# Kernel optimization log

Hardware: AMD Instinct MI355X
Metric: run time of the kernel (lower is better)

The kernel has to match this reference:

```python
import jax, jax.numpy as jnp
import numpy as np
from jax import lax

C_IN, C_OUT, K = 32, 64, 3
SUPPORT_LEN, ORDER = 1, 2
GC_IN = (ORDER * SUPPORT_LEN + 1) * C_IN  # 96
N, V, T = 32, 500, 96


def _conv2d_1xk(x, w, b):
    # x: (N,C,V,T), w: (O,I,1,K), valid padding -> (N,O,V,T-K+1)
    y = lax.conv_general_dilated(x, w, window_strides=(1, 1), padding='VALID',
                                 dimension_numbers=('NCHW', 'OIHW', 'NCHW'))
    return y + b[None, :, None, None]


def setup_inputs() -> dict:
    key = jax.random.key(0)
    ks = jax.random.split(key, 12)
    x = jax.random.normal(ks[0], (N, C_IN, V, T), dtype=jnp.float32)
    A = jax.random.uniform(ks[1], (V, V), dtype=jnp.float32)
    A = A / jnp.sum(A, axis=1, keepdims=True)  # random-walk normalization
    s = 1.0 / np.sqrt(C_IN * K)
    w1 = jax.random.uniform(ks[2], (C_IN, C_IN, 1, K), jnp.float32, -s, s)
    b1 = jax.random.uniform(ks[3], (C_IN,), jnp.float32, -s, s)
    w2 = jax.random.uniform(ks[4], (C_IN, C_IN, 1, K), jnp.float32, -s, s)
    b2 = jax.random.uniform(ks[5], (C_IN,), jnp.float32, -s, s)
    w3 = jax.random.uniform(ks[6], (C_IN, C_IN, 1, K), jnp.float32, -s, s)
    b3 = jax.random.uniform(ks[7], (C_IN,), jnp.float32, -s, s)
    so = 1.0 / np.sqrt(GC_IN)
    w_out = jax.random.uniform(ks[8], (C_OUT, GC_IN), jnp.float32, -so, so)
    b_out = jax.random.uniform(ks[9], (C_OUT,), jnp.float32, -so, so)
    prelu_a = jnp.asarray(0.25, dtype=jnp.float32)
    return {"x": x, "A": A, "w1": w1, "b1": b1, "w2": w2, "b2": b2,
            "w3": w3, "b3": b3, "w_out": w_out, "b_out": b_out,
            "prelu_a": prelu_a}


def reference(x, A, w1, b1, w2, b2, w3, b3, w_out, b_out, prelu_a):
    # TimeBlock: gated temporal conv with residual-relu
    temp = _conv2d_1xk(x, w1, b1) + jax.nn.sigmoid(_conv2d_1xk(x, w2, b2))
    xt = jax.nn.relu(temp + _conv2d_1xk(x, w3, b3))  # (N,C,V,T-2)
    # gcn: multi-hop diffusion, order=2, single support
    x1 = jnp.einsum('ncvl,vw->ncwl', xt, A)
    x2 = jnp.einsum('ncvl,vw->ncwl', x1, A)
    h = jnp.concatenate([xt, x1, x2], axis=1)  # (N,3C,V,T-2)
    # 1x1 conv projection
    out = jnp.einsum('ncvl,oc->novl', h, w_out) + b_out[None, :, None, None]
    # PReLU (scalar parameter); dropout is a no-op (training=self.training, eval)
    out = jnp.where(out > 0, out, prelu_a * out)
    return out
```

## Files before the change

### kernel.cpp

```cpp
#include <hip/hip_runtime.h>
#include <stdint.h>


typedef float  f32x4  __attribute__((ext_vector_type(4)));
typedef float  f32x2  __attribute__((ext_vector_type(2)));
typedef short  bf16x8 __attribute__((ext_vector_type(8)));

static __device__ __forceinline__ unsigned short f2bf(float f) {
    union { float f; unsigned u; } v; v.f = f;
    unsigned u = v.u;
    return (unsigned short)((u + 0x7fffu + ((u >> 16) & 1u)) >> 16);
}

#define WS_S   ((size_t)1024 * 64 * 96 * 8 * 2)
#define AT_B   (512u * 512u * 2u)
#define WA_B   (3u * 96u * 32u * 2u)

static __device__ __forceinline__ int swz(int row, int q) {
    return q ^ (row & 3) ^ ((row >> 2) & 3);
}

__global__ __launch_bounds__(256)
void prep_kernel(const float* __restrict__ A,
                 const float* __restrict__ w1, const float* __restrict__ w2,
                 const float* __restrict__ w3, const float* __restrict__ wout,
                 unsigned short* __restrict__ At, unsigned short* __restrict__ Wa,
                 unsigned short* __restrict__ Wo)
{
    int idx = blockIdx.x * 256 + threadIdx.x;
    if (idx < 512 * 512) {
        int w = idx >> 9, v = idx & 511;
        float val = (w < 500 && v < 500) ? A[v * 500 + w] : 0.f;
        At[idx] = f2bf(val);
    } else if (idx < 512 * 512 + 3 * 3 * 32 * 32) {
        int t = idx - 512 * 512;
        int ci = t & 31;
        int co = (t >> 5) & 31;
        int rc = t >> 10;
        int conv = rc % 3, koff = rc / 3;
        const float* ws = (conv == 0) ? w1 : ((conv == 1) ? w2 : w3);
        Wa[t] = f2bf(ws[co * 96 + ci * 3 + koff]);
    } else if (idx < 512 * 512 + 3 * 3 * 32 * 32 + 64 * 96) {
        int t = idx - (512 * 512 + 3 * 3 * 32 * 32);
        Wo[t] = f2bf(wout[t]);
    }
}

__global__ __launch_bounds__(512, 1)
void conv_kernel(const float* __restrict__ x, const unsigned short* __restrict__ Wa,
                 const float* __restrict__ b1, const float* __restrict__ b2,
                 const float* __restrict__ b3, unsigned short* __restrict__ xt)
{
    __shared__ unsigned short Xs2[52 * 256];
    __shared__ unsigned short WaSh[9216];
    __shared__ unsigned short stash[32 * 408];

    const int th   = blockIdx.x;
    const int vblk = blockIdx.y;
    const int n    = blockIdx.z;
    const int tid  = threadIdx.x;
    const int lane = tid & 63, wv = tid >> 6;
    const int cl = lane & 15, q4 = lane >> 4;
    const int nbase = wv * 48;

    for (int g = tid; g < 1152; g += 512)
        *(uint4*)&WaSh[g * 8] = *(const uint4*)(Wa + g * 8);

    for (int s = 0; s < 2; ++s) {
        int fid = tid + s * 512;
        if (fid < 832) {
            int rq = fid / 13, seg = fid % 13;
            int vv = rq & 7, i4 = rq >> 3;
            int v = vblk * 8 + vv;
            int tbase = th * 48 + seg * 4;
            float b[4][4];
            #pragma unroll
            for (int di = 0; di < 4; ++di) {
                float4 f = make_float4(0.f, 0.f, 0.f, 0.f);
                if (v < 500 && tbase < 96)
                    f = *(const float4*)(x + (((size_t)n * 32 + i4 * 4 + di) * 500 + v) * 96 + tbase);
                b[di][0] = f.x; b[di][1] = f.y; b[di][2] = f.z; b[di][3] = f.w;
            }
            #pragma unroll
            for (int j = 0; j < 4; ++j) {
                uint2 u;
                u.x = (unsigned)f2bf(b[0][j]) | ((unsigned)f2bf(b[1][j]) << 16);
                u.y = (unsigned)f2bf(b[2][j]) | ((unsigned)f2bf(b[3][j]) << 16);
                *(uint2*)&Xs2[(seg * 4 + j) * 256 + vv * 32 + i4 * 4] = u;
            }
        }
    }

    float bb1[2][4], bb2[2][4], bb3[2][4];
    #pragma unroll
    for (int p = 0; p < 2; ++p)
        #pragma unroll
        for (int r = 0; r < 4; ++r) {
            int c = p * 16 + q4 * 4 + r;
            bb1[p][r] = b1[c]; bb2[p][r] = b2[c]; bb3[p][r] = b3[c];
        }

    __syncthreads();

    bf16x8 af[6][3];
    #pragma unroll
    for (int mt = 0; mt < 6; ++mt)
        #pragma unroll
        for (int ko = 0; ko < 3; ++ko)
            af[mt][ko] = *(const bf16x8*)&WaSh[ko * 3072 + (mt * 16 + cl) * 32 + q4 * 8];

    f32x4 acc[6][3];
    #pragma unroll
    for (int mt = 0; mt < 6; ++mt)
        #pragma unroll
        for (int nt = 0; nt < 3; ++nt)
            acc[mt][nt] = (f32x4){0.f, 0.f, 0.f, 0.f};

    #pragma unroll
    for (int ko = 0; ko < 3; ++ko) {
        #pragma unroll
        for (int nt = 0; nt < 3; ++nt) {
            int col = nbase + nt * 16 + cl;
            int ll = col >> 3, vv = col & 7;
            bf16x8 bf = *(const bf16x8*)&Xs2[(ll + ko) * 256 + vv * 32 + q4 * 8];
            #pragma unroll
            for (int mt = 0; mt < 6; ++mt)
                acc[mt][nt] = __builtin_amdgcn_mfma_f32_16x16x32_bf16(
                    af[mt][ko], bf, acc[mt][nt], 0, 0, 0);
        }
    }

    #pragma unroll
    for (int p = 0; p < 2; ++p) {
        #pragma unroll
        for (int nt = 0; nt < 3; ++nt) {
            int col = nbase + nt * 16 + cl;
            int ll = col >> 3, vv = col & 7;
            bool valid = (th * 48 + ll) < 94;
            #pragma unroll
            for (int r = 0; r < 4; ++r) {
                float a0 = acc[p][nt][r];
                float a1 = acc[2 + p][nt][r];
                float a2 = acc[4 + p][nt][r];
                float sg = 1.f / (1.f + __expf(-(a1 + bb2[p][r])));
                float o  = fmaxf(a0 + bb1[p][r] + sg + a2 + bb3[p][r], 0.f);
                int c = p * 16 + q4 * 4 + r;
                stash[c * 408 + ll * 8 + vv] = valid ? f2bf(o) : (unsigned short)0;
            }
        }
    }
    __syncthreads();

    for (int g = tid; g < 1536; g += 512) {
        int c = g / 48, sg = g % 48;
        uint4 val = *(const uint4*)&stash[c * 408 + sg * 8];
        *(uint4*)(xt + ((((size_t)n * 32 + c) * 64 + vblk) * 96 + th * 48) * 8 + sg * 8) = val;
    }
}

__global__ __launch_bounds__(256)
void hop_kernel(const unsigned short* __restrict__ At,
                const unsigned short* __restrict__ src,
                unsigned short* __restrict__ dst)
{
    __shared__ unsigned short Ash[128 * 4 * 8];
    __shared__ unsigned short Bsh[96 * 4 * 8];

    const int mtile = blockIdx.x;
    const int b = blockIdx.y;
    const int tid = threadIdx.x;
    const int lane = tid & 63, wv = tid >> 6;
    const int mhalf = (wv & 1) * 64, nhalf = (wv >> 1) * 48;
    const int col = lane & 15, q4 = lane >> 4;

    f32x4 acc[4][3];
    #pragma unroll
    for (int mt = 0; mt < 4; ++mt)
        #pragma unroll
        for (int nt = 0; nt < 3; ++nt)
            acc[mt][nt] = (f32x4){0.f, 0.f, 0.f, 0.f};

    const unsigned short* Abase = At + (size_t)(mtile * 128) * 512;
    const unsigned short* Bbase = src + (size_t)b * 64 * 96 * 8;

    for (int kc = 0; kc < 16; ++kc) {
        __syncthreads();
        #pragma unroll
        for (int t2 = 0; t2 < 2; ++t2) {
            int idx = tid + t2 * 256;
            int r = idx >> 2, q = idx & 3;
            uint4 val = *(const uint4*)(Abase + (size_t)r * 512 + kc * 32 + q * 8);
            *(uint4*)&Ash[(r * 4 + swz(r, q)) * 8] = val;
        }
        for (int g = tid; g < 384; g += 256) {
            int q = g / 96, l = g % 96;
            uint4 val = *(const uint4*)(Bbase + ((size_t)(kc * 4 + q) * 96 + l) * 8);
            *(uint4*)&Bsh[(l * 4 + swz(l, q)) * 8] = val;
        }
        __syncthreads();

        bf16x8 af[4], bfr[3];
        #pragma unroll
        for (int mt = 0; mt < 4; ++mt) {
            int r = mhalf + mt * 16 + col;
            af[mt] = *(const bf16x8*)&Ash[(r * 4 + swz(r, q4)) * 8];
        }
        #pragma unroll
        for (int nt = 0; nt < 3; ++nt) {
            int l = nhalf + nt * 16 + col;
            bfr[nt] = *(const bf16x8*)&Bsh[(l * 4 + swz(l, q4)) * 8];
        }
        #pragma unroll
        for (int mt = 0; mt < 4; ++mt)
            #pragma unroll
            for (int nt = 0; nt < 3; ++nt)
                acc[mt][nt] = __builtin_amdgcn_mfma_f32_16x16x32_bf16(
                    af[mt], bfr[nt], acc[mt][nt], 0, 0, 0);
    }

    #pragma unroll
    for (int mt = 0; mt < 4; ++mt) {
        int w0 = mtile * 128 + mhalf + mt * 16 + q4 * 4;
        int vblk = w0 >> 3, vv0 = w0 & 7;
        #pragma unroll
        for (int nt = 0; nt < 3; ++nt) {
            int l = nhalf + nt * 16 + col;
            uint2 u;
            u.x = (unsigned)f2bf(acc[mt][nt].x) | ((unsigned)f2bf(acc[mt][nt].y) << 16);
            u.y = (unsigned)f2bf(acc[mt][nt].z) | ((unsigned)f2bf(acc[mt][nt].w) << 16);
            *(uint2*)(dst + (((size_t)b * 64 + vblk) * 96 + l) * 8 + vv0) = u;
        }
    }
}

__global__ __launch_bounds__(256)
void proj_kernel(const unsigned short* __restrict__ Wo,
                 const unsigned short* __restrict__ xt,
                 const unsigned short* __restrict__ x1,
                 const unsigned short* __restrict__ x2,
                 const float* __restrict__ bout,
                 const float* __restrict__ prelu_a,
                 float* __restrict__ out)
{
    __shared__ unsigned short WoSh[64 * 12 * 8];
    __shared__ unsigned short Bsh[128 * 4 * 8];

    const int lq = blockIdx.x;
    const int vblk = blockIdx.y;
    const int n = blockIdx.z;
    const int tid = threadIdx.x;
    const int lane = tid & 63, wv = tid >> 6;
    const int nbase = wv * 32;
    const int colL = lane & 15, q4 = lane >> 4;

    for (int g = tid; g < 768; g += 256) {
        int o = g / 12, slot = g % 12;
        int kc = slot >> 2, qq = slot & 3;
        uint4 val = *(const uint4*)(Wo + o * 96 + slot * 8);
        *(uint4*)&WoSh[(o * 12 + kc * 4 + swz(o, qq)) * 8] = val;
    }

    f32x4 acc[4][2];
    #pragma unroll
    for (int mt = 0; mt < 4; ++mt) { acc[mt][0] = (f32x4){0.f,0.f,0.f,0.f}; acc[mt][1] = (f32x4){0.f,0.f,0.f,0.f}; }

    const unsigned short* planes[3] = {xt, x1, x2};
    for (int kc = 0; kc < 3; ++kc) {
        __syncthreads();
        const unsigned short* P = planes[kc];
        #pragma unroll
        for (int t2 = 0; t2 < 2; ++t2) {
            int idx = tid + t2 * 256;
            int cl = idx >> 4, ll = idx & 15;
            union { uint4 u; unsigned short s[8]; } val;
            val.u = *(const uint4*)(P + (((size_t)(n * 32 + cl)) * 64 + vblk) * 96 * 8
                                      + (size_t)(lq * 16 + ll) * 8);
            int cq = cl >> 3, cw = cl & 7;
            #pragma unroll
            for (int vv = 0; vv < 8; ++vv) {
                int colv = vv * 16 + ll;
                Bsh[(colv * 4 + swz(colv, cq)) * 8 + cw] = val.s[vv];
            }
        }
        __syncthreads();

        bf16x8 af[4], bfr[2];
        #pragma unroll
        for (int mt = 0; mt < 4; ++mt) {
            int o = mt * 16 + colL;
            af[mt] = *(const bf16x8*)&WoSh[(o * 12 + kc * 4 + swz(o, q4)) * 8];
        }
        #pragma unroll
        for (int nt = 0; nt < 2; ++nt) {
            int colv = nbase + nt * 16 + colL;
            bfr[nt] = *(const bf16x8*)&Bsh[(colv * 4 + swz(colv, q4)) * 8];
        }
        #pragma unroll
        for (int mt = 0; mt < 4; ++mt)
            #pragma unroll
            for (int nt = 0; nt < 2; ++nt)
                acc[mt][nt] = __builtin_amdgcn_mfma_f32_16x16x32_bf16(
                    af[mt], bfr[nt], acc[mt][nt], 0, 0, 0);
    }

    const float pa = prelu_a[0];
    #pragma unroll
    for (int mt = 0; mt < 4; ++mt) {
        #pragma unroll
        for (int nt = 0; nt < 2; ++nt) {
            #pragma unroll
            for (int r = 0; r < 4; ++r) {
                int o = mt * 16 + q4 * 4 + r;
                int colv = nbase + nt * 16 + colL;
                int vv = colv >> 4, ll = colv & 15;
                int v = vblk * 8 + vv, l = lq * 16 + ll;
                if (v < 500 && l < 94) {
                    float val = acc[mt][nt][r] + bout[o];
                    val = (val > 0.f) ? val : pa * val;
                    out[(((size_t)n * 64 + o) * 500 + v) * 94 + l] = val;
                }
            }
        }
    }
}

extern "C" void kernel_launch(void* const* d_in, const int* in_sizes, int n_in,
                              void* d_out, int out_size, void* d_ws, size_t ws_size,
                              hipStream_t stream)
{
    const float* x    = (const float*)d_in[0];
    const float* A    = (const float*)d_in[1];
    const float* w1   = (const float*)d_in[2];
    const float* b1   = (const float*)d_in[3];
    const float* w2   = (const float*)d_in[4];
    const float* b2   = (const float*)d_in[5];
    const float* w3   = (const float*)d_in[6];
    const float* b3   = (const float*)d_in[7];
    const float* wout = (const float*)d_in[8];
    const float* bout = (const float*)d_in[9];
    const float* pa   = (const float*)d_in[10];
    float* out = (float*)d_out;

    char* ws = (char*)d_ws;
    unsigned short* xt = (unsigned short*)(ws);
    unsigned short* x1 = (unsigned short*)(ws + WS_S);
    unsigned short* x2 = (unsigned short*)(ws + 2 * WS_S);
    unsigned short* At = (unsigned short*)(ws + 3 * WS_S);
    unsigned short* Wa = (unsigned short*)(ws + 3 * WS_S + AT_B);
    unsigned short* Wo = (unsigned short*)(ws + 3 * WS_S + AT_B + WA_B);

    const int prep_elems = 512 * 512 + 3 * 3 * 32 * 32 + 64 * 96;
    prep_kernel<<<dim3((prep_elems + 255) / 256), 256, 0, stream>>>(
        A, w1, w2, w3, wout, At, Wa, Wo);
    conv_kernel<<<dim3(2, 63, 32), 512, 0, stream>>>(x, Wa, b1, b2, b3, xt);
    hop_kernel<<<dim3(4, 1024), 256, 0, stream>>>(At, xt, x1);
    hop_kernel<<<dim3(4, 1024), 256, 0, stream>>>(At, x1, x2);
    proj_kernel<<<dim3(6, 63, 32), 256, 0, stream>>>(Wo, xt, x1, x2, bout, pa, out);
}
```

Before: 1.038 ms.

## Remap hop blocks for XCD locality and widen proj tiles to full time rows

The hop kernel switches to a 1D grid and remaps block IDs so that blocks landing on the same XCD (round-robin by bid&7) process contiguous batch slices, with all four M-tiles of a batch on one XCD. This is meant to improve L2 reuse of the source plane. The projection kernel now uses 512 threads per block, each block covering all 96 time steps for one vblk, and each wave handles one vertex row. This enlarges the MFMA tile per wave (4x6) and writes contiguous output rows, at the cost of more LDS and registers.

```diff
diff --git a/kernel.cpp b/kernel.cpp
--- a/kernel.cpp
+++ b/kernel.cpp
@@ -166,8 +166,11 @@
     __shared__ unsigned short Ash[128 * 4 * 8];
     __shared__ unsigned short Bsh[96 * 4 * 8];
 
-    const int mtile = blockIdx.x;
-    const int b = blockIdx.y;
+    const int bid = blockIdx.x;
+    const int xcd = bid & 7;
+    const int s = bid >> 3;
+    const int mtile = s & 3;
+    const int b = xcd * 128 + (s >> 2);
     const int tid = threadIdx.x;
     const int lane = tid & 63, wv = tid >> 6;
     const int mhalf = (wv & 1) * 64, nhalf = (wv >> 1) * 48;
@@ -233,7 +236,7 @@
     }
 }
 
-__global__ __launch_bounds__(256)
+__global__ __launch_bounds__(512, 1)
 void proj_kernel(const unsigned short* __restrict__ Wo,
                  const unsigned short* __restrict__ xt,
                  const unsigned short* __restrict__ x1,
@@ -243,81 +246,85 @@
                  float* __restrict__ out)
 {
     __shared__ unsigned short WoSh[64 * 12 * 8];
-    __shared__ unsigned short Bsh[128 * 4 * 8];
-
-    const int lq = blockIdx.x;
-    const int vblk = blockIdx.y;
-    const int n = blockIdx.z;
+    __shared__ unsigned short Bsh[768 * 4 * 8];
+
+    const int vblk = blockIdx.x;
+    const int n = blockIdx.y;
     const int tid = threadIdx.x;
     const int lane = tid & 63, wv = tid >> 6;
-    const int nbase = wv * 32;
     const int colL = lane & 15, q4 = lane >> 4;
 
-    for (int g = tid; g < 768; g += 256) {
+    for (int g = tid; g < 768; g += 512) {
         int o = g / 12, slot = g % 12;
         int kc = slot >> 2, qq = slot & 3;
         uint4 val = *(const uint4*)(Wo + o * 96 + slot * 8);
         *(uint4*)&WoSh[(o * 12 + kc * 4 + swz(o, qq)) * 8] = val;
     }
 
-    f32x4 acc[4][2];
-    #pragma unroll
-    for (int mt = 0; mt < 4; ++mt) { acc[mt][0] = (f32x4){0.f,0.f,0.f,0.f}; acc[mt][1] = (f32x4){0.f,0.f,0.f,0.f}; }
+    f32x4 acc[4][6];
+    #pragma unroll
+    for (int mt = 0; mt < 4; ++mt)
+        #pragma unroll
+        for (int nt = 0; nt < 6; ++nt)
+            acc[mt][nt] = (f32x4){0.f, 0.f, 0.f, 0.f};
 
     const unsigned short* planes[3] = {xt, x1, x2};
     for (int kc = 0; kc < 3; ++kc) {
         __syncthreads();
         const unsigned short* P = planes[kc];
         #pragma unroll
-        for (int t2 = 0; t2 < 2; ++t2) {
-            int idx = tid + t2 * 256;
-            int cl = idx >> 4, ll = idx & 15;
-            union { uint4 u; unsigned short s[8]; } val;
+        for (int s = 0; s < 6; ++s) {
+            int idx = tid + s * 512;
+            int cl = idx / 96, l = idx % 96;
+            union { uint4 u; unsigned short sh[8]; } val;
             val.u = *(const uint4*)(P + (((size_t)(n * 32 + cl)) * 64 + vblk) * 96 * 8
-                                      + (size_t)(lq * 16 + ll) * 8);
+                                      + (size_t)l * 8);
             int cq = cl >> 3, cw = cl & 7;
             #pragma unroll
             for (int vv = 0; vv < 8; ++vv) {
-                int colv = vv * 16 + ll;
-                Bsh[(colv * 4 + swz(colv, cq)) * 8 + cw] = val.s[vv];
+                int colv = vv * 96 + l;
+                Bsh[(colv * 4 + swz(colv, cq)) * 8 + cw] = val.sh[vv];
             }
         }
         __syncthreads();
 
-        bf16x8 af[4], bfr[2];
+        bf16x8 af[4], bfr[6];
         #pragma unroll
         for (int mt = 0; mt < 4; ++mt) {
             int o = mt * 16 + colL;
             af[mt] = *(const bf16x8*)&WoSh[(o * 12 + kc * 4 + swz(o, q4)) * 8];
         }
         #pragma unroll
-        for (int nt = 0; nt < 2; ++nt) {
-            int colv = nbase + nt * 16 + colL;
+        for (int nt = 0; nt < 6; ++nt) {
+            int colv = wv * 96 + nt * 16 + colL;
             bfr[nt] = *(const bf16x8*)&Bsh[(colv * 4 + swz(colv, q4)) * 8];
         }
         #pragma unroll
         for (int mt = 0; mt < 4; ++mt)
             #pragma unroll
-            for (int nt = 0; nt < 2; ++nt)
+            for (int nt = 0; nt < 6; ++nt)
                 acc[mt][nt] = __builtin_amdgcn_mfma_f32_16x16x32_bf16(
                     af[mt], bfr[nt], acc[mt][nt], 0, 0, 0);
     }
 
     const float pa = prelu_a[0];
-    #pragma unroll
-    for (int mt = 0; mt < 4; ++mt) {
-        #pragma unroll
-        for (int nt = 0; nt < 2; ++nt) {
+    const int v = vblk * 8 + wv;
+    if (v < 500) {
+        #pragma unroll
+        for (int mt = 0; mt < 4; ++mt) {
             #pragma unroll
             for (int r = 0; r < 4; ++r) {
                 int o = mt * 16 + q4 * 4 + r;
-                int colv = nbase + nt * 16 + colL;
-                int vv = colv >> 4, ll = colv & 15;
-                int v = vblk * 8 + vv, l = lq * 16 + ll;
-                if (v < 500 && l < 94) {
-                    float val = acc[mt][nt][r] + bout[o];
-                    val = (val > 0.f) ? val : pa * val;
-                    out[(((size_t)n * 64 + o) * 500 + v) * 94 + l] = val;
+                float bo = bout[o];
+                float* orow = out + (((size_t)n * 64 + o) * 500 + v) * 94;
+                #pragma unroll
+                for (int nt = 0; nt < 6; ++nt) {
+                    int l = nt * 16 + colL;
+                    if (l < 94) {
+                        float val = acc[mt][nt][r] + bo;
+                        val = (val > 0.f) ? val : pa * val;
+                        orow[l] = val;
+                    }
                 }
             }
         }
@@ -353,7 +360,7 @@
     prep_kernel<<<dim3((prep_elems + 255) / 256), 256, 0, stream>>>(
         A, w1, w2, w3, wout, At, Wa, Wo);
     conv_kernel<<<dim3(2, 63, 32), 512, 0, stream>>>(x, Wa, b1, b2, b3, xt);
-    hop_kernel<<<dim3(4, 1024), 256, 0, stream>>>(At, xt, x1);
-    hop_kernel<<<dim3(4, 1024), 256, 0, stream>>>(At, x1, x2);
-    proj_kernel<<<dim3(6, 63, 32), 256, 0, stream>>>(Wo, xt, x1, x2, bout, pa, out);
-}
+    hop_kernel<<<dim3(4096), 256, 0, stream>>>(At, xt, x1);
+    hop_kernel<<<dim3(4096), 256, 0, stream>>>(At, x1, x2);
+    proj_kernel<<<dim3(63, 32), 512, 0, stream>>>(Wo, xt, x1, x2, bout, pa, out);
+}
```

Measured after the change: 922.9 us. 11.1% less time.
